# Kernel tuning notes

Hardware: AMD Instinct MI355X
Metric: run time of the kernel (lower is better)

Reference implementation:

```python
import jax, jax.numpy as jnp
import numpy as np

B, K, D, H, A = 8192, 10, 64, 128, 16
E = K * (K - 1)
# lexicographic ordered pairs (i,j), i != j -- matches adj.nonzero() and sorted(Dict.keys())
_PAIRS = np.array([(i, j) for i in range(K) for j in range(K) if i != j], dtype=np.int32)
SRC = jnp.asarray(_PAIRS[:, 0])  # message for edge (i,j) is aggregated at node i (row)
DST = jnp.asarray(_PAIRS[:, 1])


def setup_inputs() -> dict:
    key = jax.random.key(0)
    k1, k2, k3, k4, k5, k6 = jax.random.split(key, 6)
    F = D + H + A  # node MLP input dim
    return {
        "states": jax.random.normal(k1, (B, K, D), jnp.float32),
        "action_vec": jax.random.normal(k2, (B, K, A), jnp.float32),
        # one Linear(2D -> H) per ordered pair, stacked [E, 2D, H]
        "W_edge": jax.random.normal(k3, (E, 2 * D, H), jnp.float32) * (1.0 / np.sqrt(2 * D)),
        "b_edge": jax.random.normal(k4, (E, H), jnp.float32) * 0.01,
        # one Linear(D+H+A -> D) per node, stacked [K, F, D]
        "W_node": jax.random.normal(k5, (K, F, D), jnp.float32) * (1.0 / np.sqrt(F)),
        "b_node": jax.random.normal(k6, (K, D), jnp.float32) * 0.01,
    }


def reference(states, action_vec, W_edge, b_edge, W_node, b_node):
    # states: [B,K,D], action_vec: [B,K,A]
    b, k, d = states.shape
    # gather endpoints per ordered edge: [B,E,2D]
    pair_feat = jnp.concatenate([states[:, SRC, :], states[:, DST, :]], axis=-1)
    # per-edge-type Linear + tanh, batched as one grouped GEMM: [B,E,H]
    msg = jnp.tanh(jnp.einsum('bef,efh->beh', pair_feat, W_edge) + b_edge)
    # unsorted_segment_sum over source node index (row): [B,K,H]
    agg = jnp.zeros((b, k, msg.shape[-1]), msg.dtype).at[:, SRC, :].add(msg)
    # node input: [x, action, agg] -> per-node Linear + tanh: [B,K,D]
    node_in = jnp.concatenate([states, action_vec, agg], axis=-1)
    out = jnp.tanh(jnp.einsum('bkf,kfd->bkd', node_in, W_node) + b_node)
    return out
```

## Files before the change

kernel.cpp:

```cpp
#include <hip/hip_runtime.h>

typedef _Float16 f16;
typedef _Float16 f16x4 __attribute__((ext_vector_type(4)));
typedef _Float16 f16x8 __attribute__((ext_vector_type(8)));
typedef float    f32x4 __attribute__((ext_vector_type(4)));

#define S2C 2.88539008177792681472f

#define OFF_ST16 0u
#define OFF_AC16 5242880u
#define OFF_WEF  6553600u
#define OFF_WNF  8028160u
#define OFF_BE2  8171520u

__device__ __forceinline__ float fast_exp2(float x){
#if __has_builtin(__builtin_amdgcn_exp2f)
    return __builtin_amdgcn_exp2f(x);
#else
    return exp2f(x);
#endif
}
__device__ __forceinline__ float fast_rcp(float x){
#if __has_builtin(__builtin_amdgcn_rcpf)
    return __builtin_amdgcn_rcpf(x);
#else
    return 1.0f/x;
#endif
}

__device__ __forceinline__ void gl_lds16(const f16* g, f16* l){
    __builtin_amdgcn_global_load_lds(
        (const __attribute__((address_space(1))) unsigned int*)g,
        (__attribute__((address_space(3))) unsigned int*)l, 16, 0, 0);
}

#define MFMA16(a,b,c) __builtin_amdgcn_mfma_f32_16x16x32_f16(a,b,c,0,0,0)

__global__ void prep(const float* __restrict__ st, const float* __restrict__ ac,
                     const float* __restrict__ We, const float* __restrict__ be,
                     const float* __restrict__ Wn, const float* __restrict__ bn,
                     f16* __restrict__ ws16){
    const int bid = blockIdx.x, t = threadIdx.x;
    if (bid < 5120){
        int g = bid*256 + t;
        const float4 v = ((const float4*)st)[g];
        f16x4 h; h[0]=(f16)v.x; h[1]=(f16)v.y; h[2]=(f16)v.z; h[3]=(f16)v.w;
        *(f16x4*)(ws16 + OFF_ST16 + (size_t)g*4) = h;
    } else if (bid < 6400){
        int g = (bid-5120)*256 + t;
        const float4 v = ((const float4*)ac)[g];
        f16x4 h; h[0]=(f16)v.x; h[1]=(f16)v.y; h[2]=(f16)v.z; h[3]=(f16)v.w;
        *(f16x4*)(ws16 + OFF_AC16 + (size_t)g*4) = h;
    } else if (bid < 7120){
        int g = (bid-6400)*256 + t;
        int l = g & 15, q = (g>>4)&3, cg = (g>>6)&7, ks = (g>>9)&3, e = g>>11;
        const float* src = We + e*16384 + (ks*32 + q*8)*128 + cg*16 + l;
        f16x8 h;
        #pragma unroll
        for (int u=0;u<8;u++) h[u] = (f16)src[u*128];
        *(f16x8*)(ws16 + OFF_WEF + (size_t)g*8) = h;
    } else if (bid < 7190){
        int g = (bid-7120)*256 + t;
        int l = g&15, q = (g>>4)&3, c = (g>>6)&3, r = g>>8;
        int ks = r % 7, k = r / 7;
        f16x8 h;
        #pragma unroll
        for (int u=0;u<8;u++){
            int f = ks*32 + q*8 + u;
            h[u] = (f < 208) ? (f16)Wn[k*13312 + f*64 + c*16 + l] : (f16)0.0f;
        }
        *(f16x8*)(ws16 + OFF_WNF + (size_t)k*14336 + ((ks*4 + c)*64 + q*16 + l)*8) = h;
    } else {
        int g = (bid-7190)*256 + t;
        float* be2 = (float*)(ws16 + OFF_BE2);
        if (g < 11520)      be2[g] = S2C*be[g];
        else if (g < 12160) be2[g] = S2C*bn[g-11520];
    }
}

__launch_bounds__(256, 4)
__global__ void gnn_main(const f16* __restrict__ ws16, float* __restrict__ out){
    const f16* st  = ws16 + OFF_ST16;
    const f16* ac  = ws16 + OFF_AC16;
    const f16* Wef = ws16 + OFF_WEF;
    const f16* Wnf = ws16 + OFF_WNF;
    const float* be2 = (const float*)(ws16 + OFF_BE2);
    const float* bn2 = be2 + 11520;

    __shared__ alignas(16) f16 S[13312];

    const int t = threadIdx.x, lane = t&63, wid = t>>6;
    const int b0 = blockIdx.x*64;
    const int i  = blockIdx.y;
    const int l15 = lane&15, q = lane>>4, qo = q<<3;
    const int wr = (wid>>1)*32, wc = (wid&1)*64;
    const int lr = lane>>3, lc = lane&7;
    const int swz = lc ^ (lr&7);

    {
        const f16* gs = st + (size_t)b0*640 + i*64;
        #pragma unroll
        for (int it=0; it<2; ++it){
            int r0 = (wid*2+it)*8;
            gl_lds16(gs + (size_t)(r0+lr)*640 + swz*8, S + r0*64);
        }
        if (wid < 2){
            int r0 = wid*32; int row = r0 + (lane>>1); int ch = (lane&1) ^ (row&1);
            gl_lds16(ac + (size_t)(b0+row)*160 + i*16 + ch*8, S + 12288 + r0*16);
        }
        int j0 = (i==0) ? 1 : 0;
        const f16* gj = st + (size_t)b0*640 + j0*64;
        #pragma unroll
        for (int it=0; it<2; ++it){
            int r0 = (wid*2+it)*8;
            gl_lds16(gj + (size_t)(r0+lr)*640 + swz*8, S + 4096 + r0*64);
        }
    }
    __syncthreads();

    f32x4 agg[2][4] = {};

    #pragma unroll 1
    for (int e=0; e<9; ++e){
        if (e < 8){
            int j2 = (e+1) + ((e+1) >= i);
            const f16* gj = st + (size_t)b0*640 + j2*64;
            f16* dst = S + 4096 + (((e+1)&1)<<12);
            #pragma unroll
            for (int it=0; it<2; ++it){
                int r0 = (wid*2+it)*8;
                gl_lds16(gj + (size_t)(r0+lr)*640 + swz*8, dst + r0*64);
            }
        }
        const int bufb  = 4096 + ((e&1)<<12);
        const int ebase = 9*i + e;

        float bv[4];
        #pragma unroll
        for (int c=0; c<4; ++c) bv[c] = be2[ebase*128 + wc + c*16 + l15];

        f32x4 msg[2][4] = {};
        #pragma unroll
        for (int ks=0; ks<4; ++ks){
            const f16* wb = Wef + (size_t)((ebase*4 + ks)*8 + (wid&1)*4)*512 + lane*8;
            f16x8 bf[4];
            #pragma unroll
            for (int c=0; c<4; ++c) bf[c] = *(const f16x8*)(wb + c*512);
            int ab = (ks<2) ? 0 : bufb;
            int ch = (ks&1)*4 + q;
            f16x8 af[2];
            #pragma unroll
            for (int rt=0; rt<2; ++rt){
                int row = wr + rt*16 + l15;
                af[rt] = *(const f16x8*)(S + ab + row*64 + ((ch ^ (l15&7))<<3));
            }
            #pragma unroll
            for (int rt=0; rt<2; ++rt)
                #pragma unroll
                for (int c=0; c<4; ++c)
                    msg[rt][c] = MFMA16(af[rt], bf[c], msg[rt][c]);
        }
        #pragma unroll
        for (int rt=0; rt<2; ++rt)
            #pragma unroll
            for (int c=0; c<4; ++c)
                #pragma unroll
                for (int r2=0; r2<4; ++r2){
                    float tt = __builtin_fmaf(msg[rt][c][r2], S2C, bv[c]);
                    float rr = fast_rcp(fast_exp2(tt) + 1.0f);
                    agg[rt][c][r2] = __builtin_fmaf(-2.0f, rr, agg[rt][c][r2]);
                }
        __syncthreads();
    }

    #pragma unroll
    for (int rt=0; rt<2; ++rt)
        #pragma unroll
        for (int c=0; c<4; ++c)
            #pragma unroll
            for (int r2=0; r2<4; ++r2){
                int row = wr + rt*16 + q*4 + r2;
                int col = wc + c*16 + l15;
                int ch = (col>>3) ^ (row&7);
                S[4096 + row*128 + ch*8 + (col&7)] = (f16)(agg[rt][c][r2] + 9.0f);
            }
    __syncthreads();

    f32x4 acc[4] = {};
    const f16* wnb = Wnf + (size_t)i*14336;
    #pragma unroll
    for (int ks=0; ks<7; ++ks){
        int kk = ks*32 + qo;
        int row = wid*16 + l15;
        f16x8 a;
        if (kk < 64)       a = *(const f16x8*)(S + row*64 + (((kk>>3) ^ (l15&7))<<3));
        else if (kk < 80)  a = *(const f16x8*)(S + 12288 + row*16 + ((((kk-64)>>3) ^ (l15&1))<<3));
        else if (kk < 208) a = *(const f16x8*)(S + 4096 + row*128 + ((((kk-80)>>3) ^ (l15&7))<<3));
        else { f16x8 z;
               #pragma unroll
               for (int u=0;u<8;u++) z[u]=(f16)0.0f; a = z; }
        f16x8 bf[4];
        #pragma unroll
        for (int c=0; c<4; ++c)
            bf[c] = *(const f16x8*)(wnb + (size_t)((ks*4+c)*64)*8 + lane*8);
        #pragma unroll
        for (int c=0; c<4; ++c)
            acc[c] = MFMA16(a, bf[c], acc[c]);
    }
    float bnv[4];
    #pragma unroll
    for (int c=0; c<4; ++c) bnv[c] = bn2[i*64 + c*16 + l15];
    #pragma unroll
    for (int c=0; c<4; ++c)
        #pragma unroll
        for (int r2=0; r2<4; ++r2){
            int row = wid*16 + q*4 + r2;
            int col = c*16 + l15;
            float tt = __builtin_fmaf(acc[c][r2], S2C, bnv[c]);
            float rr = fast_rcp(fast_exp2(tt) + 1.0f);
            out[((size_t)(b0+row)*10 + i)*64 + col] = __builtin_fmaf(-2.0f, rr, 1.0f);
        }
}

extern "C" void kernel_launch(void* const* d_in, const int* in_sizes, int n_in,
                              void* d_out, int out_size, void* d_ws, size_t ws_size,
                              hipStream_t stream) {
    const float* states = (const float*)d_in[0];
    const float* action = (const float*)d_in[1];
    const float* W_edge = (const float*)d_in[2];
    const float* b_edge = (const float*)d_in[3];
    const float* W_node = (const float*)d_in[4];
    const float* b_node = (const float*)d_in[5];
    f16* ws16 = (f16*)d_ws;

    hipLaunchKernelGGL(prep, dim3(7238), dim3(256), 0, stream,
                       states, action, W_edge, b_edge, W_node, b_node, ws16);
    hipLaunchKernelGGL(gnn_main, dim3(128, 10), dim3(256), 0, stream,
                       ws16, (float*)d_out);
}
```

Before: 142.3 us.

## Pre-swizzle states into MFMA fragment layout and load A operands directly to registers

The prep kernel now writes states into a per-node, per-row-group MFMA fragment layout. The main kernel therefore loads A fragments straight from global memory into registers, replacing the LDS double-buffered global_load_lds staging and dropping the per-edge __syncthreads. The node-MLP weight rows are permuted so the aggregated messages come first, and the state and action fragments are read directly from global memory, with a zero buffer for padding. LDS shrinks to the aggregation buffer only and launch bounds change to 3 blocks per SM. The risk is global-load latency with no LDS reuse, since each block re-reads the j-node states and they are no longer prefetched.

```diff
diff --git a/kernel.cpp b/kernel.cpp
--- a/kernel.cpp
+++ b/kernel.cpp
@@ -7,11 +7,12 @@
 
 #define S2C 2.88539008177792681472f
 
-#define OFF_ST16 0u
-#define OFF_AC16 5242880u
+#define OFF_STF  0u
+#define OFF_AC   5242880u
 #define OFF_WEF  6553600u
 #define OFF_WNF  8028160u
 #define OFF_BE2  8171520u
+#define OFF_Z    8195840u
 
 __device__ __forceinline__ float fast_exp2(float x){
 #if __has_builtin(__builtin_amdgcn_exp2f)
@@ -28,12 +29,6 @@
 #endif
 }
 
-__device__ __forceinline__ void gl_lds16(const f16* g, f16* l){
-    __builtin_amdgcn_global_load_lds(
-        (const __attribute__((address_space(1))) unsigned int*)g,
-        (__attribute__((address_space(3))) unsigned int*)l, 16, 0, 0);
-}
-
 #define MFMA16(a,b,c) __builtin_amdgcn_mfma_f32_16x16x32_f16(a,b,c,0,0,0)
 
 __global__ void prep(const float* __restrict__ st, const float* __restrict__ ac,
@@ -41,124 +36,108 @@
                      const float* __restrict__ Wn, const float* __restrict__ bn,
                      f16* __restrict__ ws16){
     const int bid = blockIdx.x, t = threadIdx.x;
-    if (bid < 5120){
+    if (bid < 2560){
         int g = bid*256 + t;
-        const float4 v = ((const float4*)st)[g];
-        f16x4 h; h[0]=(f16)v.x; h[1]=(f16)v.y; h[2]=(f16)v.z; h[3]=(f16)v.w;
-        *(f16x4*)(ws16 + OFF_ST16 + (size_t)g*4) = h;
-    } else if (bid < 6400){
-        int g = (bid-5120)*256 + t;
+        int lane = g&63, ks = (g>>6)&1, rt = (g>>7)&1, rg2 = (g>>8)&255, node = g>>16;
+        int row = rg2*32 + rt*16 + (lane&15);
+        int k   = ks*32 + (lane>>4)*8;
+        const float* src = st + ((size_t)row*10 + node)*64 + k;
+        const float4 v0 = *(const float4*)src;
+        const float4 v1 = *(const float4*)(src+4);
+        f16x8 h; h[0]=(f16)v0.x; h[1]=(f16)v0.y; h[2]=(f16)v0.z; h[3]=(f16)v0.w;
+                 h[4]=(f16)v1.x; h[5]=(f16)v1.y; h[6]=(f16)v1.z; h[7]=(f16)v1.w;
+        *(f16x8*)(ws16 + OFF_STF + (size_t)g*8) = h;
+    } else if (bid < 3840){
+        int g = (bid-2560)*256 + t;
         const float4 v = ((const float4*)ac)[g];
         f16x4 h; h[0]=(f16)v.x; h[1]=(f16)v.y; h[2]=(f16)v.z; h[3]=(f16)v.w;
-        *(f16x4*)(ws16 + OFF_AC16 + (size_t)g*4) = h;
-    } else if (bid < 7120){
-        int g = (bid-6400)*256 + t;
+        *(f16x4*)(ws16 + OFF_AC + (size_t)g*4) = h;
+    } else if (bid < 4560){
+        int g = (bid-3840)*256 + t;
         int l = g & 15, q = (g>>4)&3, cg = (g>>6)&7, ks = (g>>9)&3, e = g>>11;
         const float* src = We + e*16384 + (ks*32 + q*8)*128 + cg*16 + l;
         f16x8 h;
         #pragma unroll
         for (int u=0;u<8;u++) h[u] = (f16)src[u*128];
         *(f16x8*)(ws16 + OFF_WEF + (size_t)g*8) = h;
-    } else if (bid < 7190){
-        int g = (bid-7120)*256 + t;
-        int l = g&15, q = (g>>4)&3, c = (g>>6)&3, r = g>>8;
-        int ks = r % 7, k = r / 7;
-        f16x8 h;
-        #pragma unroll
-        for (int u=0;u<8;u++){
-            int f = ks*32 + q*8 + u;
-            h[u] = (f < 208) ? (f16)Wn[k*13312 + f*64 + c*16 + l] : (f16)0.0f;
-        }
-        *(f16x8*)(ws16 + OFF_WNF + (size_t)k*14336 + ((ks*4 + c)*64 + q*16 + l)*8) = h;
+    } else if (bid < 4630){
+        int g = (bid-4560)*256 + t;
+        if (g < 17920){
+            int l = g&15, q=(g>>4)&3, c=(g>>6)&3, r=g>>8;
+            int ks2 = r % 7, kn = r / 7;
+            f16x8 h;
+            #pragma unroll
+            for (int u=0;u<8;u++){
+                int knew = ks2*32 + q*8 + u;
+                int f = (knew < 128) ? (knew + 80) : (knew - 128);
+                h[u] = (knew < 208) ? (f16)Wn[kn*13312 + f*64 + c*16 + l] : (f16)0.0f;
+            }
+            *(f16x8*)(ws16 + OFF_WNF + (size_t)kn*14336 + ((size_t)(ks2*4+c)*64 + q*16 + l)*8) = h;
+        }
     } else {
-        int g = (bid-7190)*256 + t;
+        int g = (bid-4630)*256 + t;
         float* be2 = (float*)(ws16 + OFF_BE2);
         if (g < 11520)      be2[g] = S2C*be[g];
         else if (g < 12160) be2[g] = S2C*bn[g-11520];
-    }
-}
-
-__launch_bounds__(256, 4)
+        else if (g < 12168) ws16[OFF_Z + (g-12160)] = (f16)0.0f;
+    }
+}
+
+__launch_bounds__(256, 3)
 __global__ void gnn_main(const f16* __restrict__ ws16, float* __restrict__ out){
-    const f16* st  = ws16 + OFF_ST16;
-    const f16* ac  = ws16 + OFF_AC16;
+    __shared__ alignas(16) f16 sAgg[64*128];
+
+    const f16* stf = ws16 + OFF_STF;
     const f16* Wef = ws16 + OFF_WEF;
-    const f16* Wnf = ws16 + OFF_WNF;
     const float* be2 = (const float*)(ws16 + OFF_BE2);
     const float* bn2 = be2 + 11520;
 
-    __shared__ alignas(16) f16 S[13312];
-
     const int t = threadIdx.x, lane = t&63, wid = t>>6;
-    const int b0 = blockIdx.x*64;
-    const int i  = blockIdx.y;
     const int l15 = lane&15, q = lane>>4, qo = q<<3;
-    const int wr = (wid>>1)*32, wc = (wid&1)*64;
-    const int lr = lane>>3, lc = lane&7;
-    const int swz = lc ^ (lr&7);
-
+    const int i  = blockIdx.x >> 7;
+    const int rb = blockIdx.x & 127;
+    const int b0 = rb*64;
+    const int rg2 = rb*2 + (wid>>1);
+    const int cs  = wid&1;
+
+    f16x8 ai[4];
     {
-        const f16* gs = st + (size_t)b0*640 + i*64;
-        #pragma unroll
-        for (int it=0; it<2; ++it){
-            int r0 = (wid*2+it)*8;
-            gl_lds16(gs + (size_t)(r0+lr)*640 + swz*8, S + r0*64);
-        }
-        if (wid < 2){
-            int r0 = wid*32; int row = r0 + (lane>>1); int ch = (lane&1) ^ (row&1);
-            gl_lds16(ac + (size_t)(b0+row)*160 + i*16 + ch*8, S + 12288 + r0*16);
-        }
-        int j0 = (i==0) ? 1 : 0;
-        const f16* gj = st + (size_t)b0*640 + j0*64;
-        #pragma unroll
-        for (int it=0; it<2; ++it){
-            int r0 = (wid*2+it)*8;
-            gl_lds16(gj + (size_t)(r0+lr)*640 + swz*8, S + 4096 + r0*64);
-        }
-    }
-    __syncthreads();
+        const f16* p = stf + (size_t)(i*256 + rg2)*2048 + lane*8;
+        ai[0] = *(const f16x8*)p;        ai[1] = *(const f16x8*)(p+512);
+        ai[2] = *(const f16x8*)(p+1024); ai[3] = *(const f16x8*)(p+1536);
+    }
 
     f32x4 agg[2][4] = {};
 
     #pragma unroll 1
     for (int e=0; e<9; ++e){
-        if (e < 8){
-            int j2 = (e+1) + ((e+1) >= i);
-            const f16* gj = st + (size_t)b0*640 + j2*64;
-            f16* dst = S + 4096 + (((e+1)&1)<<12);
-            #pragma unroll
-            for (int it=0; it<2; ++it){
-                int r0 = (wid*2+it)*8;
-                gl_lds16(gj + (size_t)(r0+lr)*640 + swz*8, dst + r0*64);
-            }
-        }
-        const int bufb  = 4096 + ((e&1)<<12);
+        const int j = e + (e >= i);
         const int ebase = 9*i + e;
 
+        f16x8 aj[4];
+        {
+            const f16* p = stf + (size_t)(j*256 + rg2)*2048 + lane*8;
+            aj[0] = *(const f16x8*)p;        aj[1] = *(const f16x8*)(p+512);
+            aj[2] = *(const f16x8*)(p+1024); aj[3] = *(const f16x8*)(p+1536);
+        }
         float bv[4];
         #pragma unroll
-        for (int c=0; c<4; ++c) bv[c] = be2[ebase*128 + wc + c*16 + l15];
+        for (int c=0; c<4; ++c) bv[c] = be2[ebase*128 + cs*64 + c*16 + l15];
 
         f32x4 msg[2][4] = {};
         #pragma unroll
-        for (int ks=0; ks<4; ++ks){
-            const f16* wb = Wef + (size_t)((ebase*4 + ks)*8 + (wid&1)*4)*512 + lane*8;
+        for (int ks4=0; ks4<4; ++ks4){
+            const f16* wb = Wef + (size_t)((ebase*4 + ks4)*8 + cs*4)*512 + lane*8;
             f16x8 bf[4];
             #pragma unroll
             for (int c=0; c<4; ++c) bf[c] = *(const f16x8*)(wb + c*512);
-            int ab = (ks<2) ? 0 : bufb;
-            int ch = (ks&1)*4 + q;
-            f16x8 af[2];
             #pragma unroll
             for (int rt=0; rt<2; ++rt){
-                int row = wr + rt*16 + l15;
-                af[rt] = *(const f16x8*)(S + ab + row*64 + ((ch ^ (l15&7))<<3));
-            }
-            #pragma unroll
-            for (int rt=0; rt<2; ++rt)
+                f16x8 a = (ks4 < 2) ? ai[rt*2 + ks4] : aj[rt*2 + (ks4-2)];
                 #pragma unroll
                 for (int c=0; c<4; ++c)
-                    msg[rt][c] = MFMA16(af[rt], bf[c], msg[rt][c]);
+                    msg[rt][c] = MFMA16(a, bf[c], msg[rt][c]);
+            }
         }
         #pragma unroll
         for (int rt=0; rt<2; ++rt)
@@ -170,7 +149,6 @@
                     float rr = fast_rcp(fast_exp2(tt) + 1.0f);
                     agg[rt][c][r2] = __builtin_fmaf(-2.0f, rr, agg[rt][c][r2]);
                 }
-        __syncthreads();
     }
 
     #pragma unroll
@@ -179,30 +157,34 @@
         for (int c=0; c<4; ++c)
             #pragma unroll
             for (int r2=0; r2<4; ++r2){
-                int row = wr + rt*16 + q*4 + r2;
-                int col = wc + c*16 + l15;
-                int ch = (col>>3) ^ (row&7);
-                S[4096 + row*128 + ch*8 + (col&7)] = (f16)(agg[rt][c][r2] + 9.0f);
+                int lrow = (wid>>1)*32 + rt*16 + q*4 + r2;
+                int col  = cs*64 + c*16 + l15;
+                sAgg[lrow*128 + (((col>>3) ^ (lrow&7))<<3) + (col&7)] = (f16)(agg[rt][c][r2] + 9.0f);
             }
     __syncthreads();
 
     f32x4 acc[4] = {};
-    const f16* wnb = Wnf + (size_t)i*14336;
-    #pragma unroll
-    for (int ks=0; ks<7; ++ks){
-        int kk = ks*32 + qo;
-        int row = wid*16 + l15;
+    const f16* wnb = ws16 + OFF_WNF + (size_t)i*14336;
+    const f16* acp = ws16 + OFF_AC;
+    const f16* zb  = ws16 + OFF_Z;
+    #pragma unroll
+    for (int ks2=0; ks2<7; ++ks2){
         f16x8 a;
-        if (kk < 64)       a = *(const f16x8*)(S + row*64 + (((kk>>3) ^ (l15&7))<<3));
-        else if (kk < 80)  a = *(const f16x8*)(S + 12288 + row*16 + ((((kk-64)>>3) ^ (l15&1))<<3));
-        else if (kk < 208) a = *(const f16x8*)(S + 4096 + row*128 + ((((kk-80)>>3) ^ (l15&7))<<3));
-        else { f16x8 z;
-               #pragma unroll
-               for (int u=0;u<8;u++) z[u]=(f16)0.0f; a = z; }
+        if (ks2 < 4){
+            int lrow = wid*16 + l15;
+            a = *(const f16x8*)(sAgg + lrow*128 + (((ks2*4 + q) ^ (l15&7))<<3));
+        } else if (ks2 < 6){
+            int fi = ((i*256 + rb*2 + (wid>>1))*2 + (wid&1))*2 + (ks2-4);
+            a = *(const f16x8*)(stf + (size_t)fi*512 + lane*8);
+        } else {
+            int row = b0 + wid*16 + l15;
+            const f16* ap = (q < 2) ? (acp + ((size_t)row*10 + i)*16 + qo) : zb;
+            a = *(const f16x8*)ap;
+        }
         f16x8 bf[4];
         #pragma unroll
         for (int c=0; c<4; ++c)
-            bf[c] = *(const f16x8*)(wnb + (size_t)((ks*4+c)*64)*8 + lane*8);
+            bf[c] = *(const f16x8*)(wnb + (size_t)(ks2*4+c)*512 + lane*8);
         #pragma unroll
         for (int c=0; c<4; ++c)
             acc[c] = MFMA16(a, bf[c], acc[c]);
@@ -214,11 +196,11 @@
     for (int c=0; c<4; ++c)
         #pragma unroll
         for (int r2=0; r2<4; ++r2){
-            int row = wid*16 + q*4 + r2;
+            int row = b0 + wid*16 + q*4 + r2;
             int col = c*16 + l15;
             float tt = __builtin_fmaf(acc[c][r2], S2C, bnv[c]);
             float rr = fast_rcp(fast_exp2(tt) + 1.0f);
-            out[((size_t)(b0+row)*10 + i)*64 + col] = __builtin_fmaf(-2.0f, rr, 1.0f);
+            out[((size_t)row*10 + i)*64 + col] = __builtin_fmaf(-2.0f, rr, 1.0f);
         }
 }
 
@@ -233,8 +215,8 @@
     const float* b_node = (const float*)d_in[5];
     f16* ws16 = (f16*)d_ws;
 
-    hipLaunchKernelGGL(prep, dim3(7238), dim3(256), 0, stream,
+    hipLaunchKernelGGL(prep, dim3(4678), dim3(256), 0, stream,
                        states, action, W_edge, b_edge, W_node, b_node, ws16);
-    hipLaunchKernelGGL(gnn_main, dim3(128, 10), dim3(256), 0, stream,
+    hipLaunchKernelGGL(gnn_main, dim3(1280), dim3(256), 0, stream,
                        ws16, (float*)d_out);
 }
```

New measurement: 156.4 us. +10.0%, slower.
